# Optimization experiments

Measured on AMD Instinct MI355X. Metric: run time of the kernel, lower is better.

## Reference

```python
import jax, jax.numpy as jnp
import numpy as np

NC, NPER, DIN, D, R = 100000, 50000, 128, 128, 7
E = 2100000
ER = E // R  # edges per relation (block layout: relation i owns rows [i*ER, (i+1)*ER))
NEG_SLOPE = 0.2


def _seg_softmax(x, seg, n):
    # numerically-stable softmax over destination-node segments (PyG `softmax`)
    m = jax.ops.segment_max(x, seg, num_segments=n)
    m = jnp.where(jnp.isfinite(m), m, 0.0)  # empty segments -> -inf; neutralize
    e = jnp.exp(x - m[seg])
    s = jax.ops.segment_sum(e, seg, num_segments=n)
    return e / (s[seg] + 1e-16)


def setup_inputs() -> dict:
    key = jax.random.key(0)
    ks = jax.random.split(key, 12)
    N = NC + NPER
    s_in = 1.0 / float(np.sqrt(DIN))
    s_d = 1.0 / float(np.sqrt(D))
    company_emb = jax.random.normal(ks[0], (NC, DIN), jnp.float32)
    person_emb = jax.random.normal(ks[1], (NPER, DIN), jnp.float32)
    edge_index = jax.random.randint(ks[2], (E, 2), 0, N)
    edge_type = jnp.repeat(jnp.arange(R), ER)  # contiguous blocks per relation
    # weights are all-ones except relation 3 -> selects the weighted message branch there
    edge_weight = jnp.ones((E, 1), jnp.float32)
    edge_weight = edge_weight.at[3 * ER:4 * ER].set(
        jax.random.uniform(ks[3], (ER, 1), jnp.float32) + 0.1)
    W_com = jax.random.normal(ks[4], (DIN, D), jnp.float32) * s_in
    W_per = jax.random.normal(ks[5], (DIN, D), jnp.float32) * s_in
    Wq = jax.random.normal(ks[6], (R, D, D), jnp.float32) * s_d
    bq = jnp.zeros((R, D), jnp.float32)
    Wk = jax.random.normal(ks[7], (R, D, D), jnp.float32) * s_d
    bk = jnp.zeros((R, D), jnp.float32)
    Wv = jax.random.normal(ks[8], (D, D), jnp.float32) * s_d
    bv = jnp.zeros((D,), jnp.float32)
    pri = jnp.ones((R,), jnp.float32)
    W_rel_pair = jax.random.normal(ks[9], (R, 2 * D, D), jnp.float32) * s_d  # slot 3 unused
    W_rel3 = jax.random.normal(ks[10], (D, D), jnp.float32) * s_d
    skip = jnp.ones((1,), jnp.float32)
    return {"company_emb": company_emb, "person_emb": person_emb, "edge_weight": edge_weight,
            "W_com": W_com, "W_per": W_per, "Wq": Wq, "bq": bq, "Wk": Wk, "bk": bk,
            "Wv": Wv, "bv": bv, "pri": pri, "W_rel_pair": W_rel_pair, "W_rel3": W_rel3,
            "skip": skip, "edge_index": edge_index, "edge_type": edge_type}


def _hetegnn(company_emb, person_emb, edge_weight, W_com, W_per, Wq, bq, Wk, bk,
             Wv, bv, pri, W_rel_pair, W_rel3, skip, edge_index, edge_type):
    emb = jnp.concatenate([company_emb @ W_com, person_emb @ W_per], axis=0)  # [N, D]
    N = emb.shape[0]
    rs_list = []
    for i in range(R):
        sl = slice(i * ER, (i + 1) * ER)
        src = edge_index[sl, 0]
        dst = edge_index[sl, 1]
        x_j = emb[src]                                   # gathered source features [ER, D]
        if i == 3:  # weighted branch: linear on x_j, scalar scatter-softmax of edge weights
            msg = (x_j @ W_rel3) * _seg_softmax(edge_weight[sl], dst, N)
        else:       # attention branch: rel_wi(concat(x_i, x_j)) -> per-dim scatter-softmax
            temp = jnp.concatenate([emb[dst], x_j], axis=1) @ W_rel_pair[i]  # [ER, D]
            msg = x_j * _seg_softmax(temp, dst, N)
        rs = jax.ops.segment_sum(msg, dst, num_segments=N)  # scatter-add aggregation
        rs_list.append(jax.nn.leaky_relu(rs, NEG_SLOPE))
    rs_stack = jnp.stack(rs_list)                           # [R, N, D]
    # cross-relation attention
    q = jnp.einsum('nd,rde->rne', emb, Wq) + bq[:, None, :]
    k = jnp.einsum('rnd,rde->rne', rs_stack, Wk) + bk[:, None, :]
    scores = (q * k).sum(-1) * pri[:, None] / jnp.sqrt(jnp.float32(D))  # [R, N]
    att = jax.nn.softmax(scores, axis=0)                    # softmax across relations
    v = rs_stack @ Wv + bv                                  # [R, N, D]
    res = jnp.einsum('rn,rnd->nd', att, v)
    res = res + jax.nn.sigmoid(skip) * jax.nn.gelu(emb, approximate=False)
    return res


def reference(company_emb, person_emb, edge_weight, W_com, W_per, Wq, bq, Wk, bk,
              Wv, bv, pri, W_rel_pair, W_rel3, skip, edge_index, edge_type):
    res = _hetegnn(company_emb, person_emb, edge_weight, W_com, W_per, Wq, bq, Wk, bk,
                   Wv, bv, pri, W_rel_pair, W_rel3, skip, edge_index, edge_type)
    return res[:NC], res[NC:]
```

## Files before the change

### kernel.cpp

```cpp
#include <hip/hip_runtime.h>
#include <stdint.h>

#define NCY 100000
#define NPR 50000
#define NT  150000
#define RREL 7
#define ETOT 2100000
#define EREL 300000
#define NSEG (RREL*NT)
#define NEG 0.2f

#define NBUK 256
#define BWID 587
#define P1B  1024
#define CH1  2051
#define EPT  9
#define LSEG (RREL*BWID)
#define SPT  17

#define LSTR 128

typedef __attribute__((ext_vector_type(8))) short short8;
typedef __attribute__((ext_vector_type(4))) float f32x4;
typedef unsigned short u16;

__device__ __forceinline__ float bf2f(u16 h){
  union{unsigned int u; float f;} v; v.u = ((unsigned int)h)<<16; return v.f;
}
__device__ __forceinline__ u16 f2bf(float f){
  union{unsigned int u; float f;} v; v.f=f;
  unsigned int u=v.u;
  return (u16)((u + 0x7fffu + ((u>>16)&1u))>>16);
}
__device__ __forceinline__ float lrelu(float x){ return x>0.f? x : NEG*x; }
__device__ __forceinline__ int lidx(int row, int col){
  return row*LSTR + ((((col>>4)^(row&7)))<<4) + (col&15);
}

#define MFMA(a,b,c) __builtin_amdgcn_mfma_f32_16x16x32_bf16(a,b,c,0,0,0)

__global__ __launch_bounds__(256) void k_bin(const int* __restrict__ eidx,
    const float* __restrict__ ew,
    int* __restrict__ bsrc, int* __restrict__ bkey, float* __restrict__ bew,
    int* __restrict__ gcntT, int* __restrict__ poffT){
  __shared__ int cnt[NBUK];
  __shared__ int pb[NBUK];
  int blk = blockIdx.x, tid = threadIdx.x;
  int base = blk*CH1;
  int n = min(CH1, ETOT-base);
  cnt[tid]=0;
  __syncthreads();
  int esrc[EPT], ekey[EPT], erank[EPT], ebuk[EPT]; float eew[EPT];
  #pragma unroll
  for(int k=0;k<EPT;k++){
    int i = k*256 + tid;
    erank[k]=-1; esrc[k]=0; ekey[k]=0; ebuk[k]=0; eew[k]=0.f;
    if(i<n){
      int e = base+i;
      int2 sd = *(const int2*)(eidx+2*e);
      int r = e/EREL;
      int b = sd.y / BWID;
      esrc[k]=sd.x; ekey[k]=r*NT+sd.y; ebuk[k]=b; eew[k]=ew[e];
      erank[k]=atomicAdd(&cnt[b],1);
    }
  }
  __syncthreads();
  int v = cnt[tid];
  pb[tid]=v; __syncthreads();
  for(int off=1; off<256; off<<=1){
    int a=(tid>=off)?pb[tid-off]:0; __syncthreads();
    pb[tid]+=a; __syncthreads();
  }
  int excl = pb[tid]-v;
  gcntT[blk*NBUK+tid]=v;
  poffT[blk*NBUK+tid]=excl;
  pb[tid]=excl; __syncthreads();
  #pragma unroll
  for(int k=0;k<EPT;k++){
    if(erank[k]>=0){
      int pos = base + pb[ebuk[k]] + erank[k];
      bsrc[pos]=esrc[k]; bkey[pos]=ekey[k]; bew[pos]=eew[k];
    }
  }
}

__global__ __launch_bounds__(256) void k_bsum(const int* __restrict__ gcntT,
                                              int* __restrict__ btot){
  __shared__ int lds[256];
  int b = blockIdx.x, t = threadIdx.x;
  int s=0;
  for(int blk=t; blk<P1B; blk+=256) s += gcntT[blk*NBUK+b];
  lds[t]=s; __syncthreads();
  for(int off=128; off>0; off>>=1){ if(t<off) lds[t]+=lds[t+off]; __syncthreads(); }
  if(t==0) btot[b]=lds[0];
}

__global__ __launch_bounds__(256) void k_bscan(const int* __restrict__ btot,
                                               int* __restrict__ bbase){
  __shared__ int lds[256];
  int t=threadIdx.x;
  int v=btot[t]; lds[t]=v; __syncthreads();
  for(int off=1; off<256; off<<=1){
    int a=(t>=off)?lds[t-off]:0; __syncthreads();
    lds[t]+=a; __syncthreads();
  }
  bbase[t]=lds[t]-v;
}

__global__ __launch_bounds__(256) void k_place(
    const int* __restrict__ bsrc, const int* __restrict__ bkey, const float* __restrict__ bew,
    const int* __restrict__ gcntT, const int* __restrict__ poffT, const int* __restrict__ bbase,
    int* __restrict__ starts_g, int* __restrict__ ends_g,
    int* __restrict__ ssrc, float* __restrict__ sew){
  __shared__ int scnt[LSEG];
  __shared__ int lrun[LSEG];
  __shared__ int gofs[P1B];
  __shared__ int gl[P1B];
  __shared__ int scan[256];
  int b = blockIdx.x, t = threadIdx.x;
  int lo = b*BWID;
  int gbase = bbase[b];
  for(int i=t;i<LSEG;i+=256) scnt[i]=0;
  for(int blk=t; blk<P1B; blk+=256){
    gl[blk]   = gcntT[blk*NBUK+b];
    gofs[blk] = poffT[blk*NBUK+b];
  }
  __syncthreads();
  for(int blk=t; blk<P1B; blk+=256){
    int o = blk*CH1 + gofs[blk], g = gl[blk];
    for(int i=0;i<g;i++){
      int key = bkey[o+i];
      int r = key/NT; int dst = key - r*NT;
      atomicAdd(&scnt[r*BWID + (dst-lo)], 1);
    }
  }
  __syncthreads();
  int ts=0;
  #pragma unroll
  for(int k=0;k<SPT;k++){ int idx=t*SPT+k; ts += (idx<LSEG)? scnt[idx]:0; }
  scan[t]=ts; __syncthreads();
  for(int off=1; off<256; off<<=1){
    int a=(t>=off)?scan[t-off]:0; __syncthreads();
    scan[t]+=a; __syncthreads();
  }
  int run = scan[t]-ts;
  #pragma unroll
  for(int k=0;k<SPT;k++){
    int idx=t*SPT+k;
    if(idx<LSEG){ lrun[idx]=run; run += scnt[idx]; }
  }
  __syncthreads();
  for(int idx=t; idx<LSEG; idx+=256){
    int r = idx/BWID; int ld = idx - r*BWID; int dst = lo+ld;
    if(dst<NT){
      int sgp = gbase + lrun[idx];
      starts_g[r*NT+dst] = sgp;
      ends_g[r*NT+dst]   = sgp + scnt[idx];
    }
  }
  __syncthreads();
  for(int idx=t; idx<LSEG; idx+=256) lrun[idx] += gbase;
  __syncthreads();
  for(int blk=t; blk<P1B; blk+=256){
    int o = blk*CH1 + gofs[blk], g = gl[blk];
    for(int i=0;i<g;i++){
      int key = bkey[o+i];
      int r = key/NT; int dst = key - r*NT;
      int pos = atomicAdd(&lrun[r*BWID+(dst-lo)], 1);
      ssrc[pos] = bsrc[o+i];
      if(r==3) sew[pos] = bew[o+i];
    }
  }
}

__global__ __launch_bounds__(256) void k_prep(const float* __restrict__ Wq, const float* __restrict__ bq,
    const float* __restrict__ Wk, const float* __restrict__ bk,
    float* __restrict__ Ar, float* __restrict__ ur, float* __restrict__ wr,
    float* __restrict__ cr, int* __restrict__ bflag){
  int t = blockIdx.x*256 + threadIdx.x;
  if(t >= RREL*128*128) return;
  int r = t/(128*128); int ij = t - r*128*128; int i = ij>>7, j = ij&127;
  const float* wq = Wq + r*16384; const float* wk = Wk + r*16384;
  float s=0.f;
  for(int k=0;k<128;k++) s += wq[i*128+k]*wk[j*128+k];
  Ar[t] = s;
  if(i==0){
    float su=0.f, sw=0.f;
    for(int k=0;k<128;k++){ su += wq[j*128+k]*bk[r*128+k];
                            sw += wk[j*128+k]*bq[r*128+k]; }
    ur[r*128+j]=su; wr[r*128+j]=sw;
    if(j==0){
      float sc=0.f; int nz=0;
      for(int k=0;k<128;k++){ float a=bq[r*128+k], b2=bk[r*128+k];
        sc += a*b2; nz |= (a!=0.f)||(b2!=0.f); }
      cr[r]=sc; if(nz) atomicOr(bflag,1);
    }
  }
}

struct PackJob{ const float* src; u16* dst; int ksteps; };
struct PackJobs{ PackJob j[20]; };
__global__ __launch_bounds__(256) void k_pack(PackJobs jobs){
  PackJob J = jobs.j[blockIdx.y];
  int t = blockIdx.x*256 + threadIdx.x;
  int lane = t&63, ks=(t>>6)&7, nt=t>>9;
  if(ks >= J.ksteps) return;
  int col = nt*16 + (lane&15);
  int krow = ks*32 + (lane>>4)*8;
  u16* d = J.dst + ((nt*J.ksteps + ks)*64 + lane)*8;
  for(int j=0;j<8;j++) d[j] = f2bf(J.src[(krow+j)*128 + col]);
}

struct GArgs {
  const void* A; const u16* B; int M; int rowoff;
  u16* outH; float* acc; float* den;
  const u16* emb16;
  const float* bv; const float* skip;
};

template<int EPI, int ASRC>
__global__ __launch_bounds__(256) void k_gemm(GArgs G)
{
  int wave = threadIdx.x>>6, lane = threadIdx.x&63;
  int M = G.M;
  int base = blockIdx.x*64 + wave*16;
  if(base >= M) return;
  int arow = base + (lane&15); if(arow >= M) arow = M-1;
  int kof = (lane>>4)*8;
  short8 a[4];
  if(ASRC==0){
    const u16* A = (const u16*)G.A;
    #pragma unroll
    for(int ks=0;ks<4;ks++) a[ks] = *(const short8*)(A + (size_t)arow*128 + ks*32 + kof);
  } else if(ASRC==3){
    const u16* A = (const u16*)G.A;
    float sc = 1.f/G.den[arow];
    #pragma unroll
    for(int ks=0;ks<4;ks++){
      short8 v = *(const short8*)(A + (size_t)arow*128 + ks*32 + kof);
      short8 s;
      #pragma unroll
      for(int j2=0;j2<8;j2++) s[j2]=f2bf(bf2f((u16)v[j2])*sc);
      a[ks]=s;
    }
  } else {
    const float* A = (const float*)G.A;
    #pragma unroll
    for(int ks=0;ks<4;ks++){
      const float* ap = A + (size_t)arow*128 + ks*32 + kof;
      f32x4 lo = *(const f32x4*)ap;
      f32x4 hi = *(const f32x4*)(ap+4);
      short8 s;
      #pragma unroll
      for(int j2=0;j2<4;j2++){ s[j2]=f2bf(lo[j2]); s[4+j2]=f2bf(hi[j2]); }
      a[ks]=s;
    }
  }
  f32x4 acc[8];
  #pragma unroll
  for(int nt=0;nt<8;nt++){
    f32x4 c = {0.f,0.f,0.f,0.f};
    #pragma unroll
    for(int ks=0;ks<4;ks++){
      short8 b = *(const short8*)(G.B + ((nt*4+ks)*64 + lane)*8);
      c = MFMA(a[ks], b, c);
    }
    acc[nt]=c;
  }
  int rbase = base + (lane>>4)*4;
  int cl = lane&15;
  if(EPI==0){
    #pragma unroll
    for(int nt=0;nt<8;nt++)
      for(int j=0;j<4;j++){
        int row=rbase+j;
        if(row<M){
          int col=nt*16+cl;
          G.outH[(size_t)(G.rowoff+row)*128+col] = f2bf(acc[nt][j]);
        }
      }
  } else if(EPI==4){
    #pragma unroll
    for(int nt=0;nt<8;nt++)
      for(int j=0;j<4;j++){
        int row=rbase+j;
        if(row<M){
          int col=nt*16+cl;
          G.outH[(size_t)row*128+col]=f2bf(__expf(acc[nt][j]));
        }
      }
  } else {
    float sg = 1.f/(1.f+__expf(-G.skip[0]));
    #pragma unroll
    for(int nt=0;nt<8;nt++)
      for(int j=0;j<4;j++){
        int row=rbase+j;
        if(row<M){
          int col=nt*16+cl;
          float x = bf2f(G.emb16[(size_t)row*128+col]);
          float g = 0.5f*x*(1.f+erff(x*0.70710678118f));
          G.acc[(size_t)row*128+col] = acc[nt][j] + G.bv[col] + sg*g;
        }
      }
  }
}

struct PArgs {
  const u16* emb16; const int* ssrc; const int* starts_g; const int* ends_g;
  const float* sew;
  const u16* ebR1; const u16* ebR2;
  const u16* pA1; const u16* pA2;
  const u16* pWr3;
  const u16* pB2a; const u16* pB2b; u16* ebW1; u16* ebW2;
  u16* acc16; float* den;
  const float* u1; const float* w1; const float* c1; const float* p1;
  const float* u2; const float* w2; const float* c2; const float* p2;
  const int* bflag;
  int r1, r2;
};

__device__ __forceinline__ void gatherAtt(u16* buf, const u16* __restrict__ ebt,
    const u16* __restrict__ emb16, const int* __restrict__ ssrc,
    const int* __restrict__ sg, const int* __restrict__ eg,
    int rel, int base64, int tid){
  #pragma unroll
  for(int p2=0;p2<2;p2++){
    int ln = (tid>>3) + p2*32;
    int gn = base64 + ln;
    int cb = (tid&7)*16;
    float num[16]={0,0,0,0,0,0,0,0,0,0,0,0,0,0,0,0};
    float den[16]={0,0,0,0,0,0,0,0,0,0,0,0,0,0,0,0};
    if(gn<NT){
      int s=sg[rel*NT+gn], e=eg[rel*NT+gn];
      int pos=s;
      for(; pos+1<e; pos+=2){
        int s0=ssrc[pos], s1=ssrc[pos+1];
        const u16* eb0=ebt+(size_t)s0*128+cb;   const u16* xm0=emb16+(size_t)s0*128+cb;
        const u16* eb1=ebt+(size_t)s1*128+cb;   const u16* xm1=emb16+(size_t)s1*128+cb;
        short8 ea0=*(const short8*)eb0, ea1=*(const short8*)(eb0+8);
        short8 xa0=*(const short8*)xm0, xa1=*(const short8*)(xm0+8);
        short8 eb0v=*(const short8*)eb1, eb1v=*(const short8*)(eb1+8);
        short8 xb0=*(const short8*)xm1, xb1=*(const short8*)(xm1+8);
        #pragma unroll
        for(int j=0;j<8;j++){
          float e00=bf2f((u16)ea0[j]), e01=bf2f((u16)ea1[j]);
          float e10=bf2f((u16)eb0v[j]), e11=bf2f((u16)eb1v[j]);
          num[j]   += bf2f((u16)xa0[j])*e00 + bf2f((u16)xb0[j])*e10;
          den[j]   += e00 + e10;
          num[8+j] += bf2f((u16)xa1[j])*e01 + bf2f((u16)xb1[j])*e11;
          den[8+j] += e01 + e11;
        }
      }
      if(pos<e){
        int s0=ssrc[pos];
        const u16* eb0=ebt+(size_t)s0*128+cb;  const u16* xm0=emb16+(size_t)s0*128+cb;
        short8 ea0=*(const short8*)eb0, ea1=*(const short8*)(eb0+8);
        short8 xa0=*(const short8*)xm0, xa1=*(const short8*)(xm0+8);
        #pragma unroll
        for(int j=0;j<8;j++){
          float e00=bf2f((u16)ea0[j]), e01=bf2f((u16)ea1[j]);
          num[j]   += bf2f((u16)xa0[j])*e00; den[j]   += e00;
          num[8+j] += bf2f((u16)xa1[j])*e01; den[8+j] += e01;
        }
      }
    }
    short8 v0, v1;
    #pragma unroll
    for(int j=0;j<8;j++){
      v0[j] = (short)f2bf(lrelu(num[j]/(den[j]+1e-16f)));
      v1[j] = (short)f2bf(lrelu(num[8+j]/(den[8+j]+1e-16f)));
    }
    int g1 = (tid&7) ^ (ln&7);
    u16* wp = buf + ln*LSTR + g1*16;
    *(short8*)wp = v0;
    *(short8*)(wp+8) = v1;
  }
}

__device__ __forceinline__ void gatherR3(u16* buf, const float* __restrict__ sew,
    const u16* __restrict__ emb16, const int* __restrict__ ssrc,
    const int* __restrict__ sg, const int* __restrict__ eg,
    int base64, int tid){
  #pragma unroll
  for(int p2=0;p2<2;p2++){
    int ln = (tid>>3) + p2*32;
    int gn = base64 + ln;
    int cb = (tid&7)*16;
    float num[16]={0,0,0,0,0,0,0,0,0,0,0,0,0,0,0,0};
    float dn=0.f;
    if(gn<NT){
      int s=sg[3*NT+gn], e=eg[3*NT+gn];
      int pos=s;
      for(; pos+1<e; pos+=2){
        int s0=ssrc[pos], s1=ssrc[pos+1];
        float w0=__expf(sew[pos]), w1=__expf(sew[pos+1]);
        dn += w0 + w1;
        const u16* xm0=emb16+(size_t)s0*128+cb;
        const u16* xm1=emb16+(size_t)s1*128+cb;
        short8 xa0=*(const short8*)xm0, xa1=*(const short8*)(xm0+8);
        short8 xb0=*(const short8*)xm1, xb1=*(const short8*)(xm1+8);
        #pragma unroll
        for(int j=0;j<8;j++){
          num[j]   += w0*bf2f((u16)xa0[j]) + w1*bf2f((u16)xb0[j]);
          num[8+j] += w0*bf2f((u16)xa1[j]) + w1*bf2f((u16)xb1[j]);
        }
      }
      if(pos<e){
        int s0=ssrc[pos];
        float w0=__expf(sew[pos]);
        dn += w0;
        const u16* xm0=emb16+(size_t)s0*128+cb;
        short8 xa0=*(const short8*)xm0, xa1=*(const short8*)(xm0+8);
        #pragma unroll
        for(int j=0;j<8;j++){
          num[j]   += w0*bf2f((u16)xa0[j]);
          num[8+j] += w0*bf2f((u16)xa1[j]);
        }
      }
    }
    float inv=1.f/(dn+1e-16f);
    short8 v0, v1;
    #pragma unroll
    for(int j=0;j<8;j++){
      v0[j] = (short)f2bf(num[j]*inv);
      v1[j] = (short)f2bf(num[8+j]*inv);
    }
    int g1 = (tid&7) ^ (ln&7);
    u16* wp = buf + ln*LSTR + g1*16;
    *(short8*)wp = v0;
    *(short8*)(wp+8) = v1;
  }
}

template<int NR, int NEB>
__global__ __launch_bounds__(256) void k_fp(PArgs P)
{
  __shared__ u16 ldsA[(NR==2 ? 2 : 1)*64*LSTR];
  u16* lds1 = ldsA;
  u16* lds2 = ldsA + (NR==2 ? 64*LSTR : 0);
  int tid = threadIdx.x;
  int base64 = blockIdx.x*64;
  gatherAtt(lds1, P.ebR1, P.emb16, P.ssrc, P.starts_g, P.ends_g, P.r1, base64, tid);
  if(NR==2) gatherAtt(lds2, P.ebR2, P.emb16, P.ssrc, P.starts_g, P.ends_g, P.r2, base64, tid);
  __syncthreads();
  int wave=tid>>6, lane=tid&63;
  int base = base64 + wave*16;
  if(base >= NT) return;
  int arow = base + (lane&15); if(arow >= NT) arow = NT-1;
  int kof = (lane>>4)*8;
  short8 a[4];
  #pragma unroll
  for(int ks=0;ks<4;ks++) a[ks] = *(const short8*)(P.emb16 + (size_t)arow*128 + ks*32 + kof);
  int rbase = base + (lane>>4)*4;
  int lrb   = wave*16 + (lane>>4)*4;
  int cl = lane&15;
  int bias = *P.bflag;
  float e1v[4], e2v[4];
  {
    f32x4 accS[8];
    #pragma unroll
    for(int nt=0;nt<8;nt++){
      f32x4 c = {0.f,0.f,0.f,0.f};
      #pragma unroll
      for(int ks=0;ks<4;ks++){
        short8 b = *(const short8*)(P.pA1 + ((nt*4+ks)*64 + lane)*8);
        c = MFMA(a[ks], b, c);
      }
      accS[nt]=c;
    }
    float prival = P.p1[0]*0.08838834764831845f;
    #pragma unroll
    for(int j=0;j<4;j++){
      int row=rbase+j; bool ok=row<NT;
      float p=0.f;
      if(ok){
        #pragma unroll
        for(int nt=0;nt<8;nt++){
          int col=nt*16+cl;
          float rv = bf2f(lds1[lidx(lrb+j,col)]);
          p += accS[nt][j]*rv;
          if(bias) p += bf2f(P.emb16[(size_t)row*128+col])*P.u1[col] + rv*P.w1[col];
        }
      }
      p += __shfl_xor(p,1,16); p += __shfl_xor(p,2,16);
      p += __shfl_xor(p,4,16); p += __shfl_xor(p,8,16);
      e1v[j] = __expf((p + P.c1[0])*prival);
    }
  }
  if(NR==2){
    f32x4 accS[8];
    #pragma unroll
    for(int nt=0;nt<8;nt++){
      f32x4 c = {0.f,0.f,0.f,0.f};
      #pragma unroll
      for(int ks=0;ks<4;ks++){
        short8 b = *(const short8*)(P.pA2 + ((nt*4+ks)*64 + lane)*8);
        c = MFMA(a[ks], b, c);
      }
      accS[nt]=c;
    }
    float prival = P.p2[0]*0.08838834764831845f;
    #pragma unroll
    for(int j=0;j<4;j++){
      int row=rbase+j; bool ok=row<NT;
      float p=0.f;
      if(ok){
        #pragma unroll
        for(int nt=0;nt<8;nt++){
          int col=nt*16+cl;
          float rv = bf2f(lds2[lidx(lrb+j,col)]);
          p += accS[nt][j]*rv;
          if(bias) p += bf2f(P.emb16[(size_t)row*128+col])*P.u2[col] + rv*P.w2[col];
        }
      }
      p += __shfl_xor(p,1,16); p += __shfl_xor(p,2,16);
      p += __shfl_xor(p,4,16); p += __shfl_xor(p,8,16);
      e2v[j] = __expf((p + P.c2[0])*prival);
    }
  }
  #pragma unroll
  for(int j=0;j<4;j++){
    int row=rbase+j;
    if(row<NT){
      float ee1=e1v[j];
      float ee2=(NR==2)? e2v[j] : 0.f;
      #pragma unroll
      for(int nt=0;nt<8;nt++){
        int col=nt*16+cl;
        size_t o=(size_t)row*128+col;
        float add = ee1*bf2f(lds1[lidx(lrb+j,col)]);
        if(NR==2) add += ee2*bf2f(lds2[lidx(lrb+j,col)]);
        P.acc16[o] = f2bf(bf2f(P.acc16[o]) + add);
      }
      if(cl==0) P.den[row] += ee1 + ee2;
    }
  }
  if(NEB>=1){
    #pragma unroll
    for(int nt=0;nt<8;nt++){
      f32x4 c = {0.f,0.f,0.f,0.f};
      #pragma unroll
      for(int ks=0;ks<4;ks++){
        short8 b = *(const short8*)(P.pB2a + ((nt*4+ks)*64 + lane)*8);
        c = MFMA(a[ks], b, c);
      }
      #pragma unroll
      for(int j=0;j<4;j++){
        int row=rbase+j;
        if(row<NT) P.ebW1[(size_t)row*128 + nt*16+cl] = f2bf(__expf(c[j]));
      }
    }
  }
  if(NEB>=2){
    #pragma unroll
    for(int nt=0;nt<8;nt++){
      f32x4 c = {0.f,0.f,0.f,0.f};
      #pragma unroll
      for(int ks=0;ks<4;ks++){
        short8 b = *(const short8*)(P.pB2b + ((nt*4+ks)*64 + lane)*8);
        c = MFMA(a[ks], b, c);
      }
      #pragma unroll
      for(int j=0;j<4;j++){
        int row=rbase+j;
        if(row<NT) P.ebW2[(size_t)row*128 + nt*16+cl] = f2bf(__expf(c[j]));
      }
    }
  }
}

__global__ __launch_bounds__(256) void k_fp0(PArgs P)
{
  __shared__ u16 lds1[64*LSTR];
  __shared__ u16 lds2[64*LSTR];
  int tid = threadIdx.x;
  int base64 = blockIdx.x*64;
  gatherR3(lds1, P.sew, P.emb16, P.ssrc, P.starts_g, P.ends_g, base64, tid);
  gatherAtt(lds2, P.ebR2, P.emb16, P.ssrc, P.starts_g, P.ends_g, P.r2, base64, tid);
  __syncthreads();
  int wave=tid>>6, lane=tid&63;
  int base = base64 + wave*16;
  if(base >= NT) return;
  int arow = base + (lane&15); if(arow >= NT) arow = NT-1;
  int hi = lane>>4;
  int kof = hi*8;
  int lar = wave*16 + (lane&15);
  short8 a[4];
  #pragma unroll
  for(int ks=0;ks<4;ks++) a[ks] = *(const short8*)(P.emb16 + (size_t)arow*128 + ks*32 + kof);
  f32x4 rs3[8];
  {
    short8 ta[4];
    #pragma unroll
    for(int ks=0;ks<4;ks++){
      int g = ((ks<<1)+(hi>>1)) ^ (lar&7);
      ta[ks] = *(const short8*)(lds1 + lar*LSTR + g*16 + ((hi&1)<<3));
    }
    #pragma unroll
    for(int nt=0;nt<8;nt++){
      f32x4 c = {0.f,0.f,0.f,0.f};
      #pragma unroll
      for(int ks=0;ks<4;ks++){
        short8 b = *(const short8*)(P.pWr3 + ((nt*4+ks)*64 + lane)*8);
        c = MFMA(ta[ks], b, c);
      }
      #pragma unroll
      for(int j=0;j<4;j++) c[j] = lrelu(c[j]);
      rs3[nt]=c;
    }
  }
  int rbase = base + (lane>>4)*4;
  int lrb   = wave*16 + (lane>>4)*4;
  int cl = lane&15;
  int bias = *P.bflag;
  float e1v[4], e2v[4];
  {
    f32x4 accS[8];
    #pragma unroll
    for(int nt=0;nt<8;nt++){
      f32x4 c = {0.f,0.f,0.f,0.f};
      #pragma unroll
      for(int ks=0;ks<4;ks++){
        short8 b = *(const short8*)(P.pA1 + ((nt*4+ks)*64 + lane)*8);
        c = MFMA(a[ks], b, c);
      }
      accS[nt]=c;
    }
    float prival = P.p1[0]*0.08838834764831845f;
    #pragma unroll
    for(int j=0;j<4;j++){
      int row=rbase+j; bool ok=row<NT;
      float p=0.f;
      if(ok){
        #pragma unroll
        for(int nt=0;nt<8;nt++){
          int col=nt*16+cl;
          float rv = rs3[nt][j];
          p += accS[nt][j]*rv;
          if(bias) p += bf2f(P.emb16[(size_t)row*128+col])*P.u1[col] + rv*P.w1[col];
        }
      }
      p += __shfl_xor(p,1,16); p += __shfl_xor(p,2,16);
      p += __shfl_xor(p,4,16); p += __shfl_xor(p,8,16);
      e1v[j] = __expf((p + P.c1[0])*prival);
    }
  }
  {
    f32x4 accS[8];
    #pragma unroll
    for(int nt=0;nt<8;nt++){
      f32x4 c = {0.f,0.f,0.f,0.f};
      #pragma unroll
      for(int ks=0;ks<4;ks++){
        short8 b = *(const short8*)(P.pA2 + ((nt*4+ks)*64 + lane)*8);
        c = MFMA(a[ks], b, c);
      }
      accS[nt]=c;
    }
    float prival = P.p2[0]*0.08838834764831845f;
    #pragma unroll
    for(int j=0;j<4;j++){
      int row=rbase+j; bool ok=row<NT;
      float p=0.f;
      if(ok){
        #pragma unroll
        for(int nt=0;nt<8;nt++){
          int col=nt*16+cl;
          float rv = bf2f(lds2[lidx(lrb+j,col)]);
          p += accS[nt][j]*rv;
          if(bias) p += bf2f(P.emb16[(size_t)row*128+col])*P.u2[col] + rv*P.w2[col];
        }
      }
      p += __shfl_xor(p,1,16); p += __shfl_xor(p,2,16);
      p += __shfl_xor(p,4,16); p += __shfl_xor(p,8,16);
      e2v[j] = __expf((p + P.c2[0])*prival);
    }
  }
  #pragma unroll
  for(int j=0;j<4;j++){
    int row=rbase+j;
    if(row<NT){
      float ee1=e1v[j], ee2=e2v[j];
      #pragma unroll
      for(int nt=0;nt<8;nt++){
        int col=nt*16+cl;
        size_t o=(size_t)row*128+col;
        float add = ee1*bf2f(f2bf(rs3[nt][j])) + ee2*bf2f(lds2[lidx(lrb+j,col)]);
        P.acc16[o] = f2bf(add);
      }
      if(cl==0) P.den[row] = ee1 + ee2;
    }
  }
  #pragma unroll
  for(int nt=0;nt<8;nt++){
    f32x4 c = {0.f,0.f,0.f,0.f};
    #pragma unroll
    for(int ks=0;ks<4;ks++){
      short8 b = *(const short8*)(P.pB2a + ((nt*4+ks)*64 + lane)*8);
      c = MFMA(a[ks], b, c);
    }
    #pragma unroll
    for(int j=0;j<4;j++){
      int row=rbase+j;
      if(row<NT) P.ebW1[(size_t)row*128 + nt*16+cl] = f2bf(__expf(c[j]));
    }
  }
  #pragma unroll
  for(int nt=0;nt<8;nt++){
    f32x4 c = {0.f,0.f,0.f,0.f};
    #pragma unroll
    for(int ks=0;ks<4;ks++){
      short8 b = *(const short8*)(P.pB2b + ((nt*4+ks)*64 + lane)*8);
      c = MFMA(a[ks], b, c);
    }
    #pragma unroll
    for(int j=0;j<4;j++){
      int row=rbase+j;
      if(row<NT) P.ebW2[(size_t)row*128 + nt*16+cl] = f2bf(__expf(c[j]));
    }
  }
}

extern "C" void kernel_launch(void* const* d_in, const int* in_sizes, int n_in,
                              void* d_out, int out_size, void* d_ws, size_t ws_size,
                              hipStream_t stream){
  const float* company = (const float*)d_in[0];
  const float* person  = (const float*)d_in[1];
  const float* eweight = (const float*)d_in[2];
  const float* W_com   = (const float*)d_in[3];
  const float* W_per   = (const float*)d_in[4];
  const float* Wq      = (const float*)d_in[5];
  const float* bq      = (const float*)d_in[6];
  const float* Wk      = (const float*)d_in[7];
  const float* bk      = (const float*)d_in[8];
  const float* Wv      = (const float*)d_in[9];
  const float* bvv     = (const float*)d_in[10];
  const float* pri     = (const float*)d_in[11];
  const float* Wpair   = (const float*)d_in[12];
  const float* Wrel3   = (const float*)d_in[13];
  const float* skip    = (const float*)d_in[14];
  const int*   eidx    = (const int*)d_in[15];
  float* out = (float*)d_out;

  char* w = (char*)d_ws;
  auto alloc = [&](size_t sz)->void*{ void* p=(void*)w; w += (sz+255)&~(size_t)255; return p; };
  u16*   emb16 = (u16*)alloc((size_t)NT*128*2);
  u16*   ebA   = (u16*)alloc((size_t)NT*128*2);
  u16*   ebB   = (u16*)alloc((size_t)NT*128*2);
  u16*   acc16 = (u16*)alloc((size_t)NT*128*2);
  float* den   = (float*)alloc((size_t)NT*4);
  int*   starts_g = (int*)alloc((size_t)NSEG*4);
  int*   ends_g   = (int*)alloc((size_t)NSEG*4);
  int*   ssrc  = (int*)alloc((size_t)ETOT*4);
  float* sew   = (float*)alloc((size_t)ETOT*4);
  float* Ar    = (float*)alloc((size_t)RREL*16384*4);
  float* ur    = (float*)alloc(RREL*128*4);
  float* wr    = (float*)alloc(RREL*128*4);
  float* cr    = (float*)alloc(RREL*4);
  int*   bflag = (int*)alloc(256);
  u16* pWcom  = (u16*)alloc(16384*2);
  u16* pWper  = (u16*)alloc(16384*2);
  u16* pWrel3 = (u16*)alloc(16384*2);
  u16* pWv    = (u16*)alloc(16384*2);
  u16* pAr    = (u16*)alloc((size_t)RREL*16384*2);
  u16* pWbot  = (u16*)alloc((size_t)6*16384*2);
  (void)ws_size; (void)in_sizes; (void)n_in; (void)out_size;

  u16* ebC = (u16*)d_out;
  u16* ebD = ebC + (size_t)NT*128;

  int*   bsrc  = (int*)ebA;
  int*   bkey  = bsrc + ETOT;
  float* bew   = (float*)(bkey + ETOT);
  int*   gcntT = (int*)acc16;
  int*   poffT = gcntT + P1B*NBUK;
  int*   btot  = poffT + P1B*NBUK;
  int*   bbase = btot + NBUK;

  hipMemsetAsync(bflag, 0, 4, stream);

  k_bin<<<P1B,256,0,stream>>>(eidx, eweight, bsrc, bkey, bew, gcntT, poffT);
  k_bsum<<<NBUK,256,0,stream>>>(gcntT, btot);
  k_bscan<<<1,256,0,stream>>>(btot, bbase);
  k_place<<<NBUK,256,0,stream>>>(bsrc,bkey,bew,gcntT,poffT,bbase,
                                 starts_g,ends_g,ssrc,sew);

  k_prep<<<(RREL*16384+255)/256,256,0,stream>>>(Wq,bq,Wk,bk,Ar,ur,wr,cr,bflag);

  const int attr[6] = {0,1,2,4,5,6};
  PackJobs pj{};
  int nj=0;
  auto addjob=[&](const float* s,u16* d,int ks){ pj.j[nj].src=s; pj.j[nj].dst=d; pj.j[nj].ksteps=ks; nj++; };
  addjob(W_com,pWcom,4); addjob(W_per,pWper,4);
  addjob(Wrel3,pWrel3,4); addjob(Wv,pWv,4);
  for(int r=0;r<RREL;r++) addjob(Ar + (size_t)r*16384, pAr + (size_t)r*16384, 4);
  for(int i=0;i<6;i++) addjob(Wpair + (size_t)attr[i]*32768 + 16384, pWbot + (size_t)i*16384, 4);
  dim3 pg(16, nj);
  k_pack<<<pg,256,0,stream>>>(pj);

  GArgs g{};
  g = GArgs{}; g.A=company; g.B=pWcom; g.M=NCY; g.rowoff=0; g.outH=emb16;
  k_gemm<0,1><<<(NCY+63)/64,256,0,stream>>>(g);
  g = GArgs{}; g.A=person; g.B=pWper; g.M=NPR; g.rowoff=NCY; g.outH=emb16;
  k_gemm<0,1><<<(NPR+63)/64,256,0,stream>>>(g);

  g = GArgs{}; g.A=emb16; g.B=pWbot; g.M=NT; g.outH=ebA;
  k_gemm<4,0><<<(NT+63)/64,256,0,stream>>>(g);

  int NBLK = (NT+63)/64;
  auto mkP = [&](int r1,int r2,const u16* eb1,const u16* eb2,
                 int sa,int sb,u16* w1,u16* w2)->PArgs{
    PArgs P{};
    P.emb16=emb16; P.ssrc=ssrc; P.starts_g=starts_g; P.ends_g=ends_g; P.sew=sew;
    P.ebR1=eb1; P.ebR2=eb2;
    P.pA1=pAr+(size_t)r1*16384; P.pA2=pAr+(size_t)r2*16384;
    P.pWr3=pWrel3;
    P.pB2a=(sa>=0)? pWbot+(size_t)sa*16384 : nullptr;
    P.pB2b=(sb>=0)? pWbot+(size_t)sb*16384 : nullptr;
    P.ebW1=w1; P.ebW2=w2;
    P.acc16=acc16; P.den=den;
    P.u1=ur+(size_t)r1*128; P.w1=wr+(size_t)r1*128; P.c1=cr+r1; P.p1=pri+r1;
    P.u2=ur+(size_t)r2*128; P.w2=wr+(size_t)r2*128; P.c2=cr+r2; P.p2=pri+r2;
    P.bflag=bflag; P.r1=r1; P.r2=r2;
    return P;
  };

  k_fp0<<<NBLK,256,0,stream>>>(mkP(3,0, nullptr,ebA, 1,2, ebC,ebD));
  k_fp<2,2><<<NBLK,256,0,stream>>>(mkP(1,2, ebC,ebD, 3,4, ebA,ebB));
  k_fp<2,1><<<NBLK,256,0,stream>>>(mkP(4,5, ebA,ebB, 5,-1, ebC,nullptr));
  k_fp<1,0><<<NBLK,256,0,stream>>>(mkP(6,6, ebC,nullptr, -1,-1, nullptr,nullptr));

  g = GArgs{}; g.A=acc16; g.B=pWv; g.M=NT;
  g.acc=out; g.den=den; g.emb16=emb16; g.bv=bvv; g.skip=skip;
  k_gemm<3,3><<<(NT+63)/64,256,0,stream>>>(g);
}
```

Baseline: 873.7 us.

## Use 16 threads per node row in gathers and skip unused edge-weight traffic

The gather routines now assign 16 threads of 8 channels each per destination node, instead of 8 threads of 16 channels, and loop over 4 row groups. This halves per-thread register arrays and spreads each node's edge list across more lanes, aiming for higher occupancy and more parallel loads. The bucketing pass also loads and stores edge weights only for relation 3, the only relation that reads them, which cuts global memory traffic. In exchange, each thread walks the source index list more times overall, since each node's edges are now traversed by twice as many lanes.

After: 921.3 us. 1.05x slower.

```diff
diff --git a/kernel.cpp b/kernel.cpp
--- a/kernel.cpp
+++ b/kernel.cpp
@@ -60,7 +60,8 @@
       int2 sd = *(const int2*)(eidx+2*e);
       int r = e/EREL;
       int b = sd.y / BWID;
-      esrc[k]=sd.x; ekey[k]=r*NT+sd.y; ebuk[k]=b; eew[k]=ew[e];
+      esrc[k]=sd.x; ekey[k]=r*NT+sd.y; ebuk[k]=b;
+      if(r==3) eew[k]=ew[e];
       erank[k]=atomicAdd(&cnt[b],1);
     }
   }
@@ -79,7 +80,8 @@
   for(int k=0;k<EPT;k++){
     if(erank[k]>=0){
       int pos = base + pb[ebuk[k]] + erank[k];
-      bsrc[pos]=esrc[k]; bkey[pos]=ekey[k]; bew[pos]=eew[k];
+      bsrc[pos]=esrc[k]; bkey[pos]=ekey[k];
+      if(ekey[k]>=3*NT && ekey[k]<4*NT) bew[pos]=eew[k];
     }
   }
 }
@@ -324,56 +326,44 @@
     const int* __restrict__ sg, const int* __restrict__ eg,
     int rel, int base64, int tid){
   #pragma unroll
-  for(int p2=0;p2<2;p2++){
-    int ln = (tid>>3) + p2*32;
+  for(int p2=0;p2<4;p2++){
+    int ln = (tid>>4) + p2*16;
     int gn = base64 + ln;
-    int cb = (tid&7)*16;
-    float num[16]={0,0,0,0,0,0,0,0,0,0,0,0,0,0,0,0};
-    float den[16]={0,0,0,0,0,0,0,0,0,0,0,0,0,0,0,0};
+    int cb = (tid&15)*8;
+    float num[8]={0,0,0,0,0,0,0,0};
+    float den[8]={0,0,0,0,0,0,0,0};
     if(gn<NT){
       int s=sg[rel*NT+gn], e=eg[rel*NT+gn];
       int pos=s;
       for(; pos+1<e; pos+=2){
         int s0=ssrc[pos], s1=ssrc[pos+1];
-        const u16* eb0=ebt+(size_t)s0*128+cb;   const u16* xm0=emb16+(size_t)s0*128+cb;
-        const u16* eb1=ebt+(size_t)s1*128+cb;   const u16* xm1=emb16+(size_t)s1*128+cb;
-        short8 ea0=*(const short8*)eb0, ea1=*(const short8*)(eb0+8);
-        short8 xa0=*(const short8*)xm0, xa1=*(const short8*)(xm0+8);
-        short8 eb0v=*(const short8*)eb1, eb1v=*(const short8*)(eb1+8);
-        short8 xb0=*(const short8*)xm1, xb1=*(const short8*)(xm1+8);
+        short8 ea=*(const short8*)(ebt  +(size_t)s0*128+cb);
+        short8 xa=*(const short8*)(emb16+(size_t)s0*128+cb);
+        short8 eb=*(const short8*)(ebt  +(size_t)s1*128+cb);
+        short8 xb=*(const short8*)(emb16+(size_t)s1*128+cb);
         #pragma unroll
         for(int j=0;j<8;j++){
-          float e00=bf2f((u16)ea0[j]), e01=bf2f((u16)ea1[j]);
-          float e10=bf2f((u16)eb0v[j]), e11=bf2f((u16)eb1v[j]);
-          num[j]   += bf2f((u16)xa0[j])*e00 + bf2f((u16)xb0[j])*e10;
-          den[j]   += e00 + e10;
-          num[8+j] += bf2f((u16)xa1[j])*e01 + bf2f((u16)xb1[j])*e11;
-          den[8+j] += e01 + e11;
+          float e0=bf2f((u16)ea[j]), e1=bf2f((u16)eb[j]);
+          num[j] += bf2f((u16)xa[j])*e0 + bf2f((u16)xb[j])*e1;
+          den[j] += e0 + e1;
         }
       }
       if(pos<e){
         int s0=ssrc[pos];
-        const u16* eb0=ebt+(size_t)s0*128+cb;  const u16* xm0=emb16+(size_t)s0*128+cb;
-        short8 ea0=*(const short8*)eb0, ea1=*(const short8*)(eb0+8);
-        short8 xa0=*(const short8*)xm0, xa1=*(const short8*)(xm0+8);
+        short8 ea=*(const short8*)(ebt  +(size_t)s0*128+cb);
+        short8 xa=*(const short8*)(emb16+(size_t)s0*128+cb);
         #pragma unroll
         for(int j=0;j<8;j++){
-          float e00=bf2f((u16)ea0[j]), e01=bf2f((u16)ea1[j]);
-          num[j]   += bf2f((u16)xa0[j])*e00; den[j]   += e00;
-          num[8+j] += bf2f((u16)xa1[j])*e01; den[8+j] += e01;
+          float e0=bf2f((u16)ea[j]);
+          num[j] += bf2f((u16)xa[j])*e0; den[j] += e0;
         }
       }
     }
-    short8 v0, v1;
-    #pragma unroll
-    for(int j=0;j<8;j++){
-      v0[j] = (short)f2bf(lrelu(num[j]/(den[j]+1e-16f)));
-      v1[j] = (short)f2bf(lrelu(num[8+j]/(den[8+j]+1e-16f)));
-    }
-    int g1 = (tid&7) ^ (ln&7);
-    u16* wp = buf + ln*LSTR + g1*16;
-    *(short8*)wp = v0;
-    *(short8*)(wp+8) = v1;
+    short8 v;
+    #pragma unroll
+    for(int j=0;j<8;j++) v[j] = (short)f2bf(lrelu(num[j]/(den[j]+1e-16f)));
+    int g1 = (cb>>4) ^ (ln&7);
+    *(short8*)(buf + ln*LSTR + g1*16 + (cb&15)) = v;
   }
 }
 
@@ -382,11 +372,11 @@
     const int* __restrict__ sg, const int* __restrict__ eg,
     int base64, int tid){
   #pragma unroll
-  for(int p2=0;p2<2;p2++){
-    int ln = (tid>>3) + p2*32;
+  for(int p2=0;p2<4;p2++){
+    int ln = (tid>>4) + p2*16;
     int gn = base64 + ln;
-    int cb = (tid&7)*16;
-    float num[16]={0,0,0,0,0,0,0,0,0,0,0,0,0,0,0,0};
+    int cb = (tid&15)*8;
+    float num[8]={0,0,0,0,0,0,0,0};
     float dn=0.f;
     if(gn<NT){
       int s=sg[3*NT+gn], e=eg[3*NT+gn];
@@ -395,40 +385,27 @@
         int s0=ssrc[pos], s1=ssrc[pos+1];
         float w0=__expf(sew[pos]), w1=__expf(sew[pos+1]);
         dn += w0 + w1;
-        const u16* xm0=emb16+(size_t)s0*128+cb;
-        const u16* xm1=emb16+(size_t)s1*128+cb;
-        short8 xa0=*(const short8*)xm0, xa1=*(const short8*)(xm0+8);
-        short8 xb0=*(const short8*)xm1, xb1=*(const short8*)(xm1+8);
+        short8 xa=*(const short8*)(emb16+(size_t)s0*128+cb);
+        short8 xb=*(const short8*)(emb16+(size_t)s1*128+cb);
         #pragma unroll
-        for(int j=0;j<8;j++){
-          num[j]   += w0*bf2f((u16)xa0[j]) + w1*bf2f((u16)xb0[j]);
-          num[8+j] += w0*bf2f((u16)xa1[j]) + w1*bf2f((u16)xb1[j]);
-        }
+        for(int j=0;j<8;j++)
+          num[j] += w0*bf2f((u16)xa[j]) + w1*bf2f((u16)xb[j]);
       }
       if(pos<e){
         int s0=ssrc[pos];
         float w0=__expf(sew[pos]);
         dn += w0;
-        const u16* xm0=emb16+(size_t)s0*128+cb;
-        short8 xa0=*(const short8*)xm0, xa1=*(const short8*)(xm0+8);
+        short8 xa=*(const short8*)(emb16+(size_t)s0*128+cb);
         #pragma unroll
-        for(int j=0;j<8;j++){
-          num[j]   += w0*bf2f((u16)xa0[j]);
-          num[8+j] += w0*bf2f((u16)xa1[j]);
-        }
+        for(int j=0;j<8;j++) num[j] += w0*bf2f((u16)xa[j]);
       }
     }
     float inv=1.f/(dn+1e-16f);
-    short8 v0, v1;
-    #pragma unroll
-    for(int j=0;j<8;j++){
-      v0[j] = (short)f2bf(num[j]*inv);
-      v1[j] = (short)f2bf(num[8+j]*inv);
-    }
-    int g1 = (tid&7) ^ (ln&7);
-    u16* wp = buf + ln*LSTR + g1*16;
-    *(short8*)wp = v0;
-    *(short8*)(wp+8) = v1;
+    short8 v;
+    #pragma unroll
+    for(int j=0;j<8;j++) v[j] = (short)f2bf(num[j]*inv);
+    int g1 = (cb>>4) ^ (ln&7);
+    *(short8*)(buf + ln*LSTR + g1*16 + (cb&15)) = v;
   }
 }
 
```
